# Kernel tuning notes

Hardware: AMD Instinct MI355X
Metric: run time of the kernel (lower is better)

Reference implementation:

```python
import jax, jax.numpy as jnp
import numpy as np

N_TX_RE = 32
N_SYM_RE = 8
N_SAMP = 256
SYMS_RE = jnp.array([-7.0, -5.0, -3.0, -1.0, 1.0, 3.0, 5.0, 7.0], dtype=jnp.float32)
C_SIG = 1.702  # sigmoid approximation constant for normal log-CDF


def setup_inputs() -> dict:
    key = jax.random.key(0)
    k1, k2, k3 = jax.random.split(key, 3)
    return {
        "log_qi": jax.random.normal(k1, (512, N_TX_RE, N_SYM_RE), dtype=jnp.float32),
        "G": jax.random.normal(k2, (512, 64, N_TX_RE), dtype=jnp.float32),
        "sqrt_2rho": jax.random.uniform(k3, (512,), dtype=jnp.float32),
        "alpha": jnp.ones((), dtype=jnp.float32),
    }


def _mfs_forward(log_qi, G, sqrt_2rho, alpha):
    N = log_qi.shape[0]
    # Precompute scaled channel: sqrt(2*rho) * G  -> (N, M, T)
    sG = sqrt_2rho[:, None, None] * G
    row = jnp.arange(N_TX_RE)[:, None, None]  # (T,1,1) for sample insertion mask
    keys = jax.random.split(jax.random.key(42), N_TX_RE)

    def step(lq, xs):
        key, xi = xs
        # --- construct_samples: categorical draws from current marginals q_i ---
        idx = jax.random.categorical(key, lq, axis=-1, shape=(N_SAMP, N, N_TX_RE))
        s_samp = SYMS_RE[idx]                       # (S, N, T)
        s_map = jnp.transpose(s_samp, (1, 2, 0))[..., None]  # (N, T, S, 1)
        s_map = jnp.broadcast_to(s_map, (N, N_TX_RE, N_SAMP, N_SYM_RE))
        # insert the full symbol alphabet at antenna xi
        s_map = jnp.where(row == xi, SYMS_RE, s_map)
        # --- compute_log_ps: sigmoid approximation of normal log-CDF ---
        s_mat = s_map.reshape(N, N_TX_RE, N_SAMP * N_SYM_RE)
        term = jnp.einsum('nmt,ntk->nmk', sG, s_mat)  # (N, M, S*K)
        log_p = jax.nn.log_sigmoid(C_SIG * term).sum(axis=1)  # (N, S*K)
        log_p = log_p.reshape(N, N_SAMP, N_SYM_RE)
        ex_log_qi = log_p.mean(axis=1)  # (N, K) Monte Carlo mean-field expectation
        # --- damped update of q_xi with stop-gradient on the MC estimate ---
        lq_xi = (1.0 - alpha) * lq[:, xi, :] + alpha * jax.lax.stop_gradient(ex_log_qi)
        lq_new = jnp.where(jnp.arange(N_TX_RE)[:, None] == xi, lq_xi[:, None, :], lq)
        # shift by (stopped) max for numerical stability
        lq_new = lq_new - jax.lax.stop_gradient(lq_new.max(axis=-1, keepdims=True))
        return lq_new, None

    lq_final, _ = jax.lax.scan(step, log_qi, (keys, jnp.arange(N_TX_RE)))
    return lq_final


def reference(log_qi, G, sqrt_2rho, alpha):
    return _mfs_forward(log_qi, G, sqrt_2rho, alpha)
```

## Files before the change

### kernel.cpp

```cpp
#include <hip/hip_runtime.h>
#include <stdint.h>

#define NB 512
#define NM 64
#define NT 32
#define NK 8
#define NS 256
#define LQP 9
#define SYF 36

#define ROTL(x, r) __builtin_amdgcn_alignbit((x), (x), 32 - (r))

#if __has_builtin(__builtin_amdgcn_exp2f)
#define EXP2(x) __builtin_amdgcn_exp2f(x)
#else
#define EXP2(x) exp2f(x)
#endif
#if __has_builtin(__builtin_amdgcn_logf)
#define LOG2(x) __builtin_amdgcn_logf(x)
#else
#define LOG2(x) __log2f(x)
#endif

__device__ __forceinline__ uint2 tf2x32(uint32_t k0, uint32_t k1, uint32_t x0, uint32_t x1) {
  uint32_t k2 = k0 ^ k1 ^ 0x1BD11BDAu;
#define TFRND(r) { x0 += x1; x1 = ROTL(x1, r); x1 ^= x0; }
  x0 += k0; x1 += k1;
  TFRND(13) TFRND(15) TFRND(26) TFRND(6)
  x0 += k1; x1 += k2 + 1u;
  TFRND(17) TFRND(29) TFRND(16) TFRND(24)
  x0 += k2; x1 += k0 + 2u;
  TFRND(13) TFRND(15) TFRND(26) TFRND(6)
  x0 += k0; x1 += k1 + 3u;
  TFRND(17) TFRND(29) TFRND(16) TFRND(24)
  x0 += k1; x1 += k2 + 4u;
  TFRND(13) TFRND(15) TFRND(26) TFRND(6)
  x0 += k2; x1 += k0 + 5u;
#undef TFRND
  return make_uint2(x0, x1);
}

__global__ __launch_bounds__(1024, 8) void mfs_fused(
    const float* __restrict__ log_qi, const float* __restrict__ G,
    const float* __restrict__ s2r, const float* __restrict__ alpha_p,
    float* __restrict__ lq_out) {
  __shared__ float sg[NM * NT];
  __shared__ float lqs[NT * LQP];
  __shared__ float symf[NS * SYF];
  __shared__ double red[16][NK];
  __shared__ uint32_t keys2[NT * 2];

  const int n = blockIdx.x;
  const int tid = threadIdx.x;

  {
    float s2v = s2r[n];
    float2 g2 = ((const float2*)(G + (size_t)n * NM * NT))[tid];
    ((float2*)sg)[tid] = make_float2(s2v * g2.x, s2v * g2.y);
  }
  if (tid < NT * NK) lqs[(tid >> 3) * LQP + (tid & 7)] = log_qi[(size_t)n * NT * NK + tid];
  if (tid < NT) {
    uint2 r = tf2x32(0u, 42u, 0u, (uint32_t)tid);
    keys2[2 * tid] = r.x; keys2[2 * tid + 1] = r.y;
  }
  __syncthreads();

  if (tid < NT * NK) {
    int t2 = tid >> 3;
    float vv = lqs[t2 * LQP + (tid & 7)];
    float mx = vv;
    mx = fmaxf(mx, __shfl_xor(mx, 1, 64));
    mx = fmaxf(mx, __shfl_xor(mx, 2, 64));
    mx = fmaxf(mx, __shfl_xor(mx, 4, 64));
    if (t2 > 0) lqs[t2 * LQP + (tid & 7)] = vv - mx;
  }
  __syncthreads();

  const float alpha = *alpha_p;
  const int t = tid & 31;
  const int sgrp = tid >> 5;
  const int ss = tid & 255;
  const int mg = tid >> 8;
  const float TINY = 1.17549435e-38f;
  const float K2 = 2.4554669595930158f;

  for (int xi = 0; xi < NT; ++xi) {
    uint32_t kA = keys2[2 * xi], kB = keys2[2 * xi + 1];
    float Fp[NK];
#pragma unroll
    for (int k = 0; k < NK; ++k) {
      float l = lqs[t * LQP + k];
      Fp[k] = EXP2(fmaf(l, -1.4426950408889634f, -0.5287663729448977f));
    }
    bool isxi = (t == xi);
#pragma unroll
    for (int d = 0; d < 8; ++d) {
      int s = sgrp + (d << 5);
      uint32_t p = ((uint32_t)((s * NB + n) * NT + t)) << 3;
      uint32_t best = 0xffffffffu;
#pragma unroll
      for (int k = 0; k < NK; ++k) {
        uint2 r = tf2x32(kA, kB, 0u, p + (uint32_t)k);
        uint32_t bits = r.x ^ r.y;
        float f = __uint_as_float((bits >> 9) | 0x3f800000u) - 1.0f;
        float u = fmaxf(f, TINY);
        float score = (-LOG2(u)) * Fp[k];
        uint32_t sv = (__float_as_uint(score) & ~7u) | (uint32_t)k;
        best = min(best, sv);
      }
      float bi = (float)(int)(best & 7u);
      float symval = fmaf(bi, 2.0f, -7.0f);
      symf[s * SYF + t] = isxi ? 0.0f : symval;
    }
    __syncthreads();

    const float* sgp = sg + mg * 16 * NT;
    const float* myrow = symf + ss * SYF;
    float acc[16];
#pragma unroll
    for (int mi = 0; mi < 16; ++mi) acc[mi] = 0.0f;
#pragma unroll
    for (int j = 0; j < 8; ++j) {
      float4 sp4 = *(const float4*)(myrow + 4 * j);
#pragma unroll
      for (int mi = 0; mi < 16; ++mi) {
        float4 g4 = ((const float4*)(sgp + mi * NT))[j];
        acc[mi] = fmaf(g4.x, sp4.x, acc[mi]);
        acc[mi] = fmaf(g4.y, sp4.y, acc[mi]);
        acc[mi] = fmaf(g4.z, sp4.z, acc[mi]);
        acc[mi] = fmaf(g4.w, sp4.w, acc[mi]);
      }
    }
    float lp[NK];
#pragma unroll
    for (int k = 0; k < NK; ++k) lp[k] = 0.0f;
#pragma unroll
    for (int mi = 0; mi < 16; ++mi) {
      float base2 = acc[mi] * K2;
      float c2 = sgp[mi * NT + xi] * K2;
#pragma unroll
      for (int k = 0; k < NK; ++k) {
        float zb = fmaf(c2, (float)(2 * k - 7), base2);
        float e2 = EXP2(-fabsf(zb));
        lp[k] += fminf(zb, 0.0f) - LOG2(1.0f + e2);
      }
    }

    double v[NK];
#pragma unroll
    for (int k = 0; k < NK; ++k) v[k] = (double)lp[k];
#pragma unroll
    for (int off = 32; off >= 1; off >>= 1) {
#pragma unroll
      for (int k = 0; k < NK; ++k) v[k] += __shfl_down(v[k], off, 64);
    }
    int wave = tid >> 6, lane = tid & 63;
    if (lane == 0) {
#pragma unroll
      for (int k = 0; k < NK; ++k) red[wave][k] = v[k];
    }
    __syncthreads();
    if (tid < NK) {
      double sum = 0.0;
#pragma unroll
      for (int q = 0; q < 16; ++q) sum += red[q][tid];
      float ex = (float)(sum * 0.0027076061740622863);
      float oldv = lqs[xi * LQP + tid];
      float newv = (1.0f - alpha) * oldv + alpha * ex;
      float mx = newv;
      mx = fmaxf(mx, __shfl_xor(mx, 1, 64));
      mx = fmaxf(mx, __shfl_xor(mx, 2, 64));
      mx = fmaxf(mx, __shfl_xor(mx, 4, 64));
      lqs[xi * LQP + tid] = newv - mx;
    }
    __syncthreads();
  }

  if (tid < NT * NK)
    lq_out[(size_t)n * NT * NK + tid] = lqs[(tid >> 3) * LQP + (tid & 7)];
}

extern "C" void kernel_launch(void* const* d_in, const int* in_sizes, int n_in,
                              void* d_out, int out_size, void* d_ws, size_t ws_size,
                              hipStream_t stream) {
  const float* log_qi = (const float*)d_in[0];
  const float* G      = (const float*)d_in[1];
  const float* s2r    = (const float*)d_in[2];
  const float* alpha  = (const float*)d_in[3];
  float* lq = (float*)d_out;
  mfs_fused<<<NB, 1024, 0, stream>>>(log_qi, G, s2r, alpha, lq);
}
```

Measured before the change: 2.698 ms.

## Compute channel-symbol products with bf16 MFMA using three-way split of channel

```diff
diff --git a/kernel.cpp b/kernel.cpp
--- a/kernel.cpp
+++ b/kernel.cpp
@@ -7,7 +7,8 @@
 #define NK 8
 #define NS 256
 #define LQP 9
-#define SYF 36
+#define SYB 40
+#define SGB 40
 
 #define ROTL(x, r) __builtin_amdgcn_alignbit((x), (x), 32 - (r))
 
@@ -21,6 +22,9 @@
 #else
 #define LOG2(x) __log2f(x)
 #endif
+
+typedef __attribute__((ext_vector_type(8))) short bf16x8;
+typedef __attribute__((ext_vector_type(16))) float f32x16;
 
 __device__ __forceinline__ uint2 tf2x32(uint32_t k0, uint32_t k1, uint32_t x0, uint32_t x1) {
   uint32_t k2 = k0 ^ k1 ^ 0x1BD11BDAu;
@@ -40,13 +44,21 @@
   return make_uint2(x0, x1);
 }
 
+__device__ __forceinline__ uint32_t rne_bf16(float x) {
+  uint32_t u = __float_as_uint(x);
+  return (u + 0x7fffu + ((u >> 16) & 1u)) >> 16;
+}
+
 __global__ __launch_bounds__(1024, 8) void mfs_fused(
     const float* __restrict__ log_qi, const float* __restrict__ G,
     const float* __restrict__ s2r, const float* __restrict__ alpha_p,
     float* __restrict__ lq_out) {
-  __shared__ float sg[NM * NT];
+  __shared__ float sgT[NT * NM];
+  __shared__ ushort sgh[NM * SGB];
+  __shared__ ushort sgl[NM * SGB];
+  __shared__ ushort sgl2[NM * SGB];
+  __shared__ ushort symb[NS * SYB];
   __shared__ float lqs[NT * LQP];
-  __shared__ float symf[NS * SYF];
   __shared__ double red[16][NK];
   __shared__ uint32_t keys2[NT * 2];
 
@@ -56,7 +68,23 @@
   {
     float s2v = s2r[n];
     float2 g2 = ((const float2*)(G + (size_t)n * NM * NT))[tid];
-    ((float2*)sg)[tid] = make_float2(s2v * g2.x, s2v * g2.y);
+#pragma unroll
+    for (int e = 0; e < 2; ++e) {
+      int i = 2 * tid + e;
+      int m = i >> 5, t = i & 31;
+      float x = s2v * (e ? g2.y : g2.x);
+      uint32_t h = rne_bf16(x);
+      float hf = __uint_as_float(h << 16);
+      float r1 = x - hf;
+      uint32_t l = rne_bf16(r1);
+      float lf = __uint_as_float(l << 16);
+      float r2 = r1 - lf;
+      uint32_t l2 = rne_bf16(r2);
+      sgh[m * SGB + t]  = (ushort)h;
+      sgl[m * SGB + t]  = (ushort)l;
+      sgl2[m * SGB + t] = (ushort)l2;
+      sgT[t * NM + m] = x;
+    }
   }
   if (tid < NT * NK) lqs[(tid >> 3) * LQP + (tid & 7)] = log_qi[(size_t)n * NT * NK + tid];
   if (tid < NT) {
@@ -79,8 +107,14 @@
   const float alpha = *alpha_p;
   const int t = tid & 31;
   const int sgrp = tid >> 5;
-  const int ss = tid & 255;
-  const int mg = tid >> 8;
+  const int lane = tid & 63;
+  const int wid = tid >> 6;
+  const int s_tile = wid & 7;
+  const int m_tile = wid >> 3;
+  const int lm = lane & 31;
+  const int kh = lane >> 5;
+  const int sA = s_tile * 32 + lm;
+  const int mB = m_tile * 32 + lm;
   const float TINY = 1.17549435e-38f;
   const float K2 = 2.4554669595930158f;
 
@@ -110,34 +144,31 @@
       }
       float bi = (float)(int)(best & 7u);
       float symval = fmaf(bi, 2.0f, -7.0f);
-      symf[s * SYF + t] = isxi ? 0.0f : symval;
+      symb[s * SYB + t] = isxi ? (ushort)0 : (ushort)(__float_as_uint(symval) >> 16);
     }
     __syncthreads();
 
-    const float* sgp = sg + mg * 16 * NT;
-    const float* myrow = symf + ss * SYF;
-    float acc[16];
-#pragma unroll
-    for (int mi = 0; mi < 16; ++mi) acc[mi] = 0.0f;
-#pragma unroll
-    for (int j = 0; j < 8; ++j) {
-      float4 sp4 = *(const float4*)(myrow + 4 * j);
-#pragma unroll
-      for (int mi = 0; mi < 16; ++mi) {
-        float4 g4 = ((const float4*)(sgp + mi * NT))[j];
-        acc[mi] = fmaf(g4.x, sp4.x, acc[mi]);
-        acc[mi] = fmaf(g4.y, sp4.y, acc[mi]);
-        acc[mi] = fmaf(g4.z, sp4.z, acc[mi]);
-        acc[mi] = fmaf(g4.w, sp4.w, acc[mi]);
-      }
-    }
+    f32x16 acc;
+#pragma unroll
+    for (int i = 0; i < 16; ++i) acc[i] = 0.0f;
+#pragma unroll
+    for (int c = 0; c < 2; ++c) {
+      int ko = c * 16 + kh * 8;
+      bf16x8 a   = *(const bf16x8*)(symb + sA * SYB + ko);
+      bf16x8 bh  = *(const bf16x8*)(sgh  + mB * SGB + ko);
+      bf16x8 bl  = *(const bf16x8*)(sgl  + mB * SGB + ko);
+      bf16x8 bl2 = *(const bf16x8*)(sgl2 + mB * SGB + ko);
+      acc = __builtin_amdgcn_mfma_f32_32x32x16_bf16(a, bh,  acc, 0, 0, 0);
+      acc = __builtin_amdgcn_mfma_f32_32x32x16_bf16(a, bl,  acc, 0, 0, 0);
+      acc = __builtin_amdgcn_mfma_f32_32x32x16_bf16(a, bl2, acc, 0, 0, 0);
+    }
+    float c2 = sgT[xi * NM + mB] * K2;
     float lp[NK];
 #pragma unroll
     for (int k = 0; k < NK; ++k) lp[k] = 0.0f;
 #pragma unroll
-    for (int mi = 0; mi < 16; ++mi) {
-      float base2 = acc[mi] * K2;
-      float c2 = sgp[mi * NT + xi] * K2;
+    for (int reg = 0; reg < 16; ++reg) {
+      float base2 = acc[reg] * K2;
 #pragma unroll
       for (int k = 0; k < NK; ++k) {
         float zb = fmaf(c2, (float)(2 * k - 7), base2);
@@ -154,10 +185,10 @@
 #pragma unroll
       for (int k = 0; k < NK; ++k) v[k] += __shfl_down(v[k], off, 64);
     }
-    int wave = tid >> 6, lane = tid & 63;
-    if (lane == 0) {
-#pragma unroll
-      for (int k = 0; k < NK; ++k) red[wave][k] = v[k];
+    int wv = tid >> 6, ln = tid & 63;
+    if (ln == 0) {
+#pragma unroll
+      for (int k = 0; k < NK; ++k) red[wv][k] = v[k];
     }
     __syncthreads();
     if (tid < NK) {
```

After: 2.463 ms. 1.1x faster.
